# Optimization experiments

Hardware: AMD Instinct MI355X
Metric: run time of the kernel (lower is better)

The kernel has to match this reference:

```python
import jax, jax.numpy as jnp
import numpy as np

TAU1, TAU2, TSCALE = 30.0, 5.0, 6.0   # tau1 > tau2, in frame units (hz=None)
B, T_OUT = 1000, 20000                # neurons x output frames


def _biexp_kernel():
    # exact replica of SpikeToCalcium.set_double_exp
    r = TAU1 / TAU2
    d = TAU1 - TAU2
    scale = np.power(r, -TAU2 / d) - np.power(r, -TAU1 / d)
    t = np.arange(1.0, TAU1 * TSCALE + 2.0, dtype=np.float32)  # 181 taps
    e1 = np.exp(-t / TAU1)
    e2 = np.exp(-t / TAU2)
    return ((e1 - e2) / scale).astype(np.float32)


def setup_inputs() -> dict:
    key = jax.random.key(0)
    kernel = jnp.asarray(_biexp_kernel())           # (181,)
    Kt = kernel.shape[0]
    u = jax.random.normal(key, (B, T_OUT + Kt - 1), dtype=jnp.float32)  # (1000, 20180)
    return {"u": u, "kernel": kernel}


def reference(u, kernel):
    # Original: K.conv1d(u[..., None], kernel[::-1, None, None], 1, 'valid')
    # keras conv1d is cross-correlation; reversing the kernel makes it a true
    # causal FIR convolution. lax.conv_general_dilated is also cross-correlation,
    # so we pass the reversed kernel identically.
    rhs = kernel[::-1][None, None, :]               # (O=1, I=1, K)
    lhs = u[:, None, :]                             # (B, C=1, T_in)
    out = jax.lax.conv_general_dilated(
        lhs, rhs, window_strides=(1,), padding='VALID',
        dimension_numbers=('NCH', 'OIH', 'NCH'))
    return out[:, 0, :]                             # (B, T_in - K + 1)
```

## Files before the change

kernel.cpp:

```cpp
#include <hip/hip_runtime.h>
#include <math.h>


namespace {
constexpr int kB   = 1000;
constexpr int kT   = 20000;
constexpr int kInW = kT + 180;
constexpr int W    = 180;
constexpr int L    = 836;
constexpr int NCHK = 2;
}

struct Coefs {
  float r1e[8], r2e[8];
  float s1c[6], s2c[6];
  float r1_512;
  float A1, A1d, A2;
};

__global__ __launch_bounds__(256, 8)
void biexp_iir_scan(const float* __restrict__ u, float* __restrict__ out, Coefs cf) {
  const int lane = threadIdx.x & 63;
  const int seg  = (blockIdx.x << 2) | (threadIdx.x >> 6);
  const int row  = blockIdx.y;
  const int n0   = seg * L;
  const int nend = (n0 + L < kT) ? n0 + L : kT;
  const int lim  = nend - n0 + W;
  const float* ur = u + (size_t)row * kInW;
  float* outr = out + (size_t)row * kT;

  const int colbase = n0 + 8 * lane;
  int col0 = colbase;
  col0 = col0 < (kInW - 8) ? col0 : (kInW - 8);
  int col1 = colbase + 512;
  col1 = col1 < (kInW - 8) ? col1 : (kInW - 8);
  const float4 a0 = *(const float4*)(ur + col0);
  const float4 a1 = *(const float4*)(ur + col0 + 4);
  const float4 b0 = *(const float4*)(ur + col1);
  const float4 b1 = *(const float4*)(ur + col1 + 4);

  float r1l = 1.f, r2l = 1.f;
  #pragma unroll
  for (int i = 0; i < 6; ++i) {
    r1l *= (lane & (1 << i)) ? cf.s1c[i] : 1.f;
    r2l *= (lane & (1 << i)) ? cf.s2c[i] : 1.f;
  }

  float C1 = 0.f, C2 = 0.f;
  float pw[8];
  #pragma unroll
  for (int j = 0; j < 8; ++j) pw[j] = 0.f;

  auto chunk = [&](const float4& qa, const float4& qb, int c) {
    const float ux[8] = {qa.x, qa.y, qa.z, qa.w, qb.x, qb.y, qb.z, qb.w};

    float p1[8], p2[8];
    p1[0] = ux[0]; p2[0] = ux[0];
    #pragma unroll
    for (int j = 1; j < 8; ++j) {
      p1[j] = fmaf(cf.r1e[1], p1[j-1], ux[j]);
      p2[j] = fmaf(cf.r2e[1], p2[j-1], ux[j]);
    }

    float S1 = p1[7], S2 = p2[7], t;
    t = __shfl_up(S1, 1);  S1 = lane >= 1  ? fmaf(cf.s1c[0], t, S1) : S1;
    t = __shfl_up(S2, 1);  S2 = lane >= 1  ? fmaf(cf.s2c[0], t, S2) : S2;
    t = __shfl_up(S1, 2);  S1 = lane >= 2  ? fmaf(cf.s1c[1], t, S1) : S1;
    t = __shfl_up(S2, 2);  S2 = lane >= 2  ? fmaf(cf.s2c[1], t, S2) : S2;
    t = __shfl_up(S1, 4);  S1 = lane >= 4  ? fmaf(cf.s1c[2], t, S1) : S1;
    t = __shfl_up(S2, 4);  S2 = lane >= 4  ? fmaf(cf.s2c[2], t, S2) : S2;
    t = __shfl_up(S1, 8);  S1 = lane >= 8  ? fmaf(cf.s1c[3], t, S1) : S1;
    t = __shfl_up(S2, 8);  S2 = lane >= 8  ? fmaf(cf.s2c[3], t, S2) : S2;
    t = __shfl_up(S1, 16); S1 = lane >= 16 ? fmaf(cf.s1c[4], t, S1) : S1;
    t = __shfl_up(S1, 32); S1 = lane >= 32 ? fmaf(cf.s1c[5], t, S1) : S1;

    float X1 = __shfl_up(S1, 1); X1 = (lane == 0) ? 0.f : X1;
    float X2 = __shfl_up(S2, 1); X2 = (lane == 0) ? 0.f : X2;
    const float H1 = cf.r1e[1] * fmaf(r1l, C1, X1);
    const float H2 = cf.r2e[1] * fmaf(r2l, C2, X2);

    float s1[8], s2[8];
    #pragma unroll
    for (int j = 0; j < 8; ++j) {
      s1[j] = fmaf(cf.r1e[j], H1, p1[j]);
      s2[j] = fmaf(cf.r2e[j], H2, p2[j]);
    }
    C1 = fmaf(cf.r1_512, C1, __shfl(S1, 63));
    C2 = __shfl(S2, 63);

    float y[8];
    #pragma unroll
    for (int j = 0; j < 8; ++j) {
      const int slot = (j < 5) ? j + 3 : j - 5;
      const int rot  = (j < 5) ? 23 : 22;
      const float z  = (lane <= 63 - rot) ? s1[slot] : pw[slot];
      const float d  = __shfl(z, (lane - rot) & 63);
      y[j] = fmaf(-cf.A2, s2[j], fmaf(-cf.A1d, d, cf.A1 * s1[j]));
    }
    #pragma unroll
    for (int j = 0; j < 8; ++j) pw[j] = s1[j];

    const int off0 = (c << 9) + 8 * lane;
    if (off0 >= W && off0 < lim) {
      float4 v; v.x = y[0]; v.y = y[1]; v.z = y[2]; v.w = y[3];
      *(float4*)(outr + (n0 - W + off0)) = v;
    }
    if (off0 + 4 >= W && off0 + 4 < lim) {
      float4 v; v.x = y[4]; v.y = y[5]; v.z = y[6]; v.w = y[7];
      *(float4*)(outr + (n0 - W + off0 + 4)) = v;
    }
  };

  chunk(a0, a1, 0);
  chunk(b0, b1, 1);
}

extern "C" void kernel_launch(void* const* d_in, const int* in_sizes, int n_in,
                              void* d_out, int out_size, void* d_ws, size_t ws_size,
                              hipStream_t stream) {
  const float* u = (const float*)d_in[0];
  float* out = (float*)d_out;

  const double r1 = exp(-1.0 / 30.0);
  const double r2 = exp(-1.0 / 5.0);
  const double scale = pow(6.0, -5.0 / 25.0) - pow(6.0, -30.0 / 25.0);

  Coefs cf;
  for (int j = 0; j < 8; ++j) {
    cf.r1e[j] = (float)pow(r1, (double)j);
    cf.r2e[j] = (float)pow(r2, (double)j);
  }
  for (int i = 0; i < 6; ++i) {
    cf.s1c[i] = (float)pow(r1, (double)(8 << i));
    cf.s2c[i] = (float)pow(r2, (double)(8 << i));
  }
  cf.r1_512 = (float)pow(r1, 512.0);
  cf.A1  = (float)(r1 / scale);
  cf.A1d = (float)(pow(r1, 182.0) / scale);
  cf.A2  = (float)(r2 / scale);

  hipLaunchKernelGGL(biexp_iir_scan, dim3(6, kB), dim3(256, 1, 1), 0, stream,
                     u, out, cf);
}
```

Measured before the change: 142.4 us.

## Process one 1024-sample window per wave with 16 elements per lane

Each wave now loads 16 consecutive samples per lane and covers its whole segment window in one pass, replacing the two 8-element chunks with a carried prefix. The cross-lane scan shrinks to five levels for the slow pole and three for the fast pole. The delayed-tap lookup becomes a single rotated shuffle with zero fill, and the segment length is retuned. The aim is fewer shuffles and less carried state per output, at the cost of more registers per thread (launch bounds lowered to 6) and more overlap work since segment length and window ratio change.

```diff
diff --git a/kernel.cpp b/kernel.cpp
--- a/kernel.cpp
+++ b/kernel.cpp
@@ -7,18 +7,18 @@
 constexpr int kT   = 20000;
 constexpr int kInW = kT + 180;
 constexpr int W    = 180;
-constexpr int L    = 836;
-constexpr int NCHK = 2;
+constexpr int L    = 844;
+constexpr int SEGS = 24;
 }
 
 struct Coefs {
-  float r1e[8], r2e[8];
-  float s1c[6], s2c[6];
-  float r1_512;
+  float r1e[16], r2e[16];
+  float s1c[5];
+  float s2c[3];
   float A1, A1d, A2;
 };
 
-__global__ __launch_bounds__(256, 8)
+__global__ __launch_bounds__(256, 6)
 void biexp_iir_scan(const float* __restrict__ u, float* __restrict__ out, Coefs cf) {
   const int lane = threadIdx.x & 63;
   const int seg  = (blockIdx.x << 2) | (threadIdx.x >> 6);
@@ -29,90 +29,67 @@
   const float* ur = u + (size_t)row * kInW;
   float* outr = out + (size_t)row * kT;
 
-  const int colbase = n0 + 8 * lane;
-  int col0 = colbase;
-  col0 = col0 < (kInW - 8) ? col0 : (kInW - 8);
-  int col1 = colbase + 512;
-  col1 = col1 < (kInW - 8) ? col1 : (kInW - 8);
-  const float4 a0 = *(const float4*)(ur + col0);
-  const float4 a1 = *(const float4*)(ur + col0 + 4);
-  const float4 b0 = *(const float4*)(ur + col1);
-  const float4 b1 = *(const float4*)(ur + col1 + 4);
+  int cb = n0 + 16 * lane;
+  cb = cb < (kInW - 16) ? cb : (kInW - 16);
+  const float4 q0 = *(const float4*)(ur + cb);
+  const float4 q1 = *(const float4*)(ur + cb + 4);
+  const float4 q2 = *(const float4*)(ur + cb + 8);
+  const float4 q3 = *(const float4*)(ur + cb + 12);
 
-  float r1l = 1.f, r2l = 1.f;
+  const float ux[16] = {q0.x, q0.y, q0.z, q0.w, q1.x, q1.y, q1.z, q1.w,
+                        q2.x, q2.y, q2.z, q2.w, q3.x, q3.y, q3.z, q3.w};
+
+  float p1[16], p2[16];
+  p1[0] = ux[0]; p2[0] = ux[0];
   #pragma unroll
-  for (int i = 0; i < 6; ++i) {
-    r1l *= (lane & (1 << i)) ? cf.s1c[i] : 1.f;
-    r2l *= (lane & (1 << i)) ? cf.s2c[i] : 1.f;
+  for (int j = 1; j < 16; ++j) {
+    p1[j] = fmaf(cf.r1e[1], p1[j-1], ux[j]);
+    p2[j] = fmaf(cf.r2e[1], p2[j-1], ux[j]);
   }
 
-  float C1 = 0.f, C2 = 0.f;
-  float pw[8];
+  float S1 = p1[15], S2 = p2[15], t;
+  t = __shfl_up(S1, 1);  S1 = lane >= 1  ? fmaf(cf.s1c[0], t, S1) : S1;
+  t = __shfl_up(S2, 1);  S2 = lane >= 1  ? fmaf(cf.s2c[0], t, S2) : S2;
+  t = __shfl_up(S1, 2);  S1 = lane >= 2  ? fmaf(cf.s1c[1], t, S1) : S1;
+  t = __shfl_up(S2, 2);  S2 = lane >= 2  ? fmaf(cf.s2c[1], t, S2) : S2;
+  t = __shfl_up(S1, 4);  S1 = lane >= 4  ? fmaf(cf.s1c[2], t, S1) : S1;
+  t = __shfl_up(S2, 4);  S2 = lane >= 4  ? fmaf(cf.s2c[2], t, S2) : S2;
+  t = __shfl_up(S1, 8);  S1 = lane >= 8  ? fmaf(cf.s1c[3], t, S1) : S1;
+  t = __shfl_up(S1, 16); S1 = lane >= 16 ? fmaf(cf.s1c[4], t, S1) : S1;
+
+  float X1 = __shfl_up(S1, 1); X1 = (lane == 0) ? 0.f : X1;
+  float X2 = __shfl_up(S2, 1); X2 = (lane == 0) ? 0.f : X2;
+  const float H1 = cf.r1e[1] * X1;
+  const float H2 = cf.r2e[1] * X2;
+
+  float s1[16], s2[16];
   #pragma unroll
-  for (int j = 0; j < 8; ++j) pw[j] = 0.f;
+  for (int j = 0; j < 16; ++j) {
+    s1[j] = fmaf(cf.r1e[j], H1, p1[j]);
+    s2[j] = fmaf(cf.r2e[j], H2, p2[j]);
+  }
 
-  auto chunk = [&](const float4& qa, const float4& qb, int c) {
-    const float ux[8] = {qa.x, qa.y, qa.z, qa.w, qb.x, qb.y, qb.z, qb.w};
+  float y[16];
+  #pragma unroll
+  for (int j = 0; j < 16; ++j) {
+    const int slot = (j >= 5) ? j - 5 : j + 11;
+    const int rot  = (j >= 5) ? 11 : 12;
+    const float zz = __shfl(s1[slot], (lane - rot) & 63);
+    const float d  = (lane >= rot) ? zz : 0.f;
+    y[j] = fmaf(-cf.A2, s2[j], fmaf(-cf.A1d, d, cf.A1 * s1[j]));
+  }
 
-    float p1[8], p2[8];
-    p1[0] = ux[0]; p2[0] = ux[0];
-    #pragma unroll
-    for (int j = 1; j < 8; ++j) {
-      p1[j] = fmaf(cf.r1e[1], p1[j-1], ux[j]);
-      p2[j] = fmaf(cf.r2e[1], p2[j-1], ux[j]);
+  const int off0 = 16 * lane;
+  float* op = outr + (n0 - W + off0);
+  #pragma unroll
+  for (int q = 0; q < 4; ++q) {
+    const int off = off0 + 4 * q;
+    if (off >= W && off < lim) {
+      float4 v;
+      v.x = y[4*q+0]; v.y = y[4*q+1]; v.z = y[4*q+2]; v.w = y[4*q+3];
+      *(float4*)(op + 4 * q) = v;
     }
-
-    float S1 = p1[7], S2 = p2[7], t;
-    t = __shfl_up(S1, 1);  S1 = lane >= 1  ? fmaf(cf.s1c[0], t, S1) : S1;
-    t = __shfl_up(S2, 1);  S2 = lane >= 1  ? fmaf(cf.s2c[0], t, S2) : S2;
-    t = __shfl_up(S1, 2);  S1 = lane >= 2  ? fmaf(cf.s1c[1], t, S1) : S1;
-    t = __shfl_up(S2, 2);  S2 = lane >= 2  ? fmaf(cf.s2c[1], t, S2) : S2;
-    t = __shfl_up(S1, 4);  S1 = lane >= 4  ? fmaf(cf.s1c[2], t, S1) : S1;
-    t = __shfl_up(S2, 4);  S2 = lane >= 4  ? fmaf(cf.s2c[2], t, S2) : S2;
-    t = __shfl_up(S1, 8);  S1 = lane >= 8  ? fmaf(cf.s1c[3], t, S1) : S1;
-    t = __shfl_up(S2, 8);  S2 = lane >= 8  ? fmaf(cf.s2c[3], t, S2) : S2;
-    t = __shfl_up(S1, 16); S1 = lane >= 16 ? fmaf(cf.s1c[4], t, S1) : S1;
-    t = __shfl_up(S1, 32); S1 = lane >= 32 ? fmaf(cf.s1c[5], t, S1) : S1;
-
-    float X1 = __shfl_up(S1, 1); X1 = (lane == 0) ? 0.f : X1;
-    float X2 = __shfl_up(S2, 1); X2 = (lane == 0) ? 0.f : X2;
-    const float H1 = cf.r1e[1] * fmaf(r1l, C1, X1);
-    const float H2 = cf.r2e[1] * fmaf(r2l, C2, X2);
-
-    float s1[8], s2[8];
-    #pragma unroll
-    for (int j = 0; j < 8; ++j) {
-      s1[j] = fmaf(cf.r1e[j], H1, p1[j]);
-      s2[j] = fmaf(cf.r2e[j], H2, p2[j]);
-    }
-    C1 = fmaf(cf.r1_512, C1, __shfl(S1, 63));
-    C2 = __shfl(S2, 63);
-
-    float y[8];
-    #pragma unroll
-    for (int j = 0; j < 8; ++j) {
-      const int slot = (j < 5) ? j + 3 : j - 5;
-      const int rot  = (j < 5) ? 23 : 22;
-      const float z  = (lane <= 63 - rot) ? s1[slot] : pw[slot];
-      const float d  = __shfl(z, (lane - rot) & 63);
-      y[j] = fmaf(-cf.A2, s2[j], fmaf(-cf.A1d, d, cf.A1 * s1[j]));
-    }
-    #pragma unroll
-    for (int j = 0; j < 8; ++j) pw[j] = s1[j];
-
-    const int off0 = (c << 9) + 8 * lane;
-    if (off0 >= W && off0 < lim) {
-      float4 v; v.x = y[0]; v.y = y[1]; v.z = y[2]; v.w = y[3];
-      *(float4*)(outr + (n0 - W + off0)) = v;
-    }
-    if (off0 + 4 >= W && off0 + 4 < lim) {
-      float4 v; v.x = y[4]; v.y = y[5]; v.z = y[6]; v.w = y[7];
-      *(float4*)(outr + (n0 - W + off0 + 4)) = v;
-    }
-  };
-
-  chunk(a0, a1, 0);
-  chunk(b0, b1, 1);
+  }
 }
 
 extern "C" void kernel_launch(void* const* d_in, const int* in_sizes, int n_in,
@@ -126,19 +103,16 @@
   const double scale = pow(6.0, -5.0 / 25.0) - pow(6.0, -30.0 / 25.0);
 
   Coefs cf;
-  for (int j = 0; j < 8; ++j) {
+  for (int j = 0; j < 16; ++j) {
     cf.r1e[j] = (float)pow(r1, (double)j);
     cf.r2e[j] = (float)pow(r2, (double)j);
   }
-  for (int i = 0; i < 6; ++i) {
-    cf.s1c[i] = (float)pow(r1, (double)(8 << i));
-    cf.s2c[i] = (float)pow(r2, (double)(8 << i));
-  }
-  cf.r1_512 = (float)pow(r1, 512.0);
+  for (int i = 0; i < 5; ++i) cf.s1c[i] = (float)pow(r1, (double)(16 << i));
+  for (int i = 0; i < 3; ++i) cf.s2c[i] = (float)pow(r2, (double)(16 << i));
   cf.A1  = (float)(r1 / scale);
   cf.A1d = (float)(pow(r1, 182.0) / scale);
   cf.A2  = (float)(r2 / scale);
 
-  hipLaunchKernelGGL(biexp_iir_scan, dim3(6, kB), dim3(256, 1, 1), 0, stream,
+  hipLaunchKernelGGL(biexp_iir_scan, dim3(SEGS / 4, kB), dim3(256, 1, 1), 0, stream,
                      u, out, cf);
 }
```

Result: slower. 150.9 us (+6.0%).

## Use persistent waves with next-task load prefetch and XCD-aware block remap

Applied to the files above, without the earlier changes.

Swaps the one-segment-per-wave 2D grid for a fixed grid of 2048 blocks. Each wave loops over up to three (row, segment) tasks and issues the global loads for the next task before computing the current one, with a sched_barrier to keep that ordering. Block indices are also permuted so consecutive logical blocks land across the XCDs. The goal is to hide global-load latency in this latency-bound scan, at the cost of more live registers and uneven tail work across waves.

```diff
diff --git a/kernel.cpp b/kernel.cpp
--- a/kernel.cpp
+++ b/kernel.cpp
@@ -3,12 +3,15 @@
 
 
 namespace {
-constexpr int kB   = 1000;
-constexpr int kT   = 20000;
-constexpr int kInW = kT + 180;
-constexpr int W    = 180;
-constexpr int L    = 836;
-constexpr int NCHK = 2;
+constexpr int kB    = 1000;
+constexpr int kT    = 20000;
+constexpr int kInW  = kT + 180;
+constexpr int W     = 180;
+constexpr int L     = 836;
+constexpr int SEGS  = 24;
+constexpr int NTASK = SEGS * kB;
+constexpr int NBLK  = 2048;
+constexpr int NWAVE = NBLK * 4;
 }
 
 struct Coefs {
@@ -21,23 +24,9 @@
 __global__ __launch_bounds__(256, 8)
 void biexp_iir_scan(const float* __restrict__ u, float* __restrict__ out, Coefs cf) {
   const int lane = threadIdx.x & 63;
-  const int seg  = (blockIdx.x << 2) | (threadIdx.x >> 6);
-  const int row  = blockIdx.y;
-  const int n0   = seg * L;
-  const int nend = (n0 + L < kT) ? n0 + L : kT;
-  const int lim  = nend - n0 + W;
-  const float* ur = u + (size_t)row * kInW;
-  float* outr = out + (size_t)row * kT;
 
-  const int colbase = n0 + 8 * lane;
-  int col0 = colbase;
-  col0 = col0 < (kInW - 8) ? col0 : (kInW - 8);
-  int col1 = colbase + 512;
-  col1 = col1 < (kInW - 8) ? col1 : (kInW - 8);
-  const float4 a0 = *(const float4*)(ur + col0);
-  const float4 a1 = *(const float4*)(ur + col0 + 4);
-  const float4 b0 = *(const float4*)(ur + col1);
-  const float4 b1 = *(const float4*)(ur + col1 + 4);
+  const int lbid = (blockIdx.x & 7) * (NBLK >> 3) + (blockIdx.x >> 3);
+  const int w    = (lbid << 2) | (threadIdx.x >> 6);
 
   float r1l = 1.f, r2l = 1.f;
   #pragma unroll
@@ -46,73 +35,114 @@
     r2l *= (lane & (1 << i)) ? cf.s2c[i] : 1.f;
   }
 
-  float C1 = 0.f, C2 = 0.f;
-  float pw[8];
-  #pragma unroll
-  for (int j = 0; j < 8; ++j) pw[j] = 0.f;
+  auto load_task = [&](int t, float4& a0, float4& a1, float4& b0, float4& b1) {
+    const int row = t / SEGS;
+    const int n0  = (t - row * SEGS) * L;
+    const float* ur = u + (size_t)row * kInW;
+    int c0 = n0 + 8 * lane;
+    c0 = c0 < (kInW - 8) ? c0 : (kInW - 8);
+    int c1 = n0 + 512 + 8 * lane;
+    c1 = c1 < (kInW - 8) ? c1 : (kInW - 8);
+    a0 = *(const float4*)(ur + c0);
+    a1 = *(const float4*)(ur + c0 + 4);
+    b0 = *(const float4*)(ur + c1);
+    b1 = *(const float4*)(ur + c1 + 4);
+  };
 
-  auto chunk = [&](const float4& qa, const float4& qb, int c) {
-    const float ux[8] = {qa.x, qa.y, qa.z, qa.w, qb.x, qb.y, qb.z, qb.w};
+  auto compute_store = [&](int t, const float4& qa0, const float4& qa1,
+                                  const float4& qb0, const float4& qb1) {
+    const int row  = t / SEGS;
+    const int n0   = (t - row * SEGS) * L;
+    const int nend = (n0 + L < kT) ? n0 + L : kT;
+    const int lim  = nend - n0 + W;
+    float* outr = out + (size_t)row * kT;
 
-    float p1[8], p2[8];
-    p1[0] = ux[0]; p2[0] = ux[0];
+    float C1 = 0.f, C2 = 0.f;
+    float pw[8];
     #pragma unroll
-    for (int j = 1; j < 8; ++j) {
-      p1[j] = fmaf(cf.r1e[1], p1[j-1], ux[j]);
-      p2[j] = fmaf(cf.r2e[1], p2[j-1], ux[j]);
-    }
+    for (int j = 0; j < 8; ++j) pw[j] = 0.f;
 
-    float S1 = p1[7], S2 = p2[7], t;
-    t = __shfl_up(S1, 1);  S1 = lane >= 1  ? fmaf(cf.s1c[0], t, S1) : S1;
-    t = __shfl_up(S2, 1);  S2 = lane >= 1  ? fmaf(cf.s2c[0], t, S2) : S2;
-    t = __shfl_up(S1, 2);  S1 = lane >= 2  ? fmaf(cf.s1c[1], t, S1) : S1;
-    t = __shfl_up(S2, 2);  S2 = lane >= 2  ? fmaf(cf.s2c[1], t, S2) : S2;
-    t = __shfl_up(S1, 4);  S1 = lane >= 4  ? fmaf(cf.s1c[2], t, S1) : S1;
-    t = __shfl_up(S2, 4);  S2 = lane >= 4  ? fmaf(cf.s2c[2], t, S2) : S2;
-    t = __shfl_up(S1, 8);  S1 = lane >= 8  ? fmaf(cf.s1c[3], t, S1) : S1;
-    t = __shfl_up(S2, 8);  S2 = lane >= 8  ? fmaf(cf.s2c[3], t, S2) : S2;
-    t = __shfl_up(S1, 16); S1 = lane >= 16 ? fmaf(cf.s1c[4], t, S1) : S1;
-    t = __shfl_up(S1, 32); S1 = lane >= 32 ? fmaf(cf.s1c[5], t, S1) : S1;
+    #pragma unroll
+    for (int c = 0; c < 2; ++c) {
+      const float4& qa = c ? qb0 : qa0;
+      const float4& qb = c ? qb1 : qa1;
+      const float ux[8] = {qa.x, qa.y, qa.z, qa.w, qb.x, qb.y, qb.z, qb.w};
 
-    float X1 = __shfl_up(S1, 1); X1 = (lane == 0) ? 0.f : X1;
-    float X2 = __shfl_up(S2, 1); X2 = (lane == 0) ? 0.f : X2;
-    const float H1 = cf.r1e[1] * fmaf(r1l, C1, X1);
-    const float H2 = cf.r2e[1] * fmaf(r2l, C2, X2);
+      float p1[8], p2[8];
+      p1[0] = ux[0]; p2[0] = ux[0];
+      #pragma unroll
+      for (int j = 1; j < 8; ++j) {
+        p1[j] = fmaf(cf.r1e[1], p1[j-1], ux[j]);
+        p2[j] = fmaf(cf.r2e[1], p2[j-1], ux[j]);
+      }
 
-    float s1[8], s2[8];
-    #pragma unroll
-    for (int j = 0; j < 8; ++j) {
-      s1[j] = fmaf(cf.r1e[j], H1, p1[j]);
-      s2[j] = fmaf(cf.r2e[j], H2, p2[j]);
-    }
-    C1 = fmaf(cf.r1_512, C1, __shfl(S1, 63));
-    C2 = __shfl(S2, 63);
+      float S1 = p1[7], S2 = p2[7], t_;
+      t_ = __shfl_up(S1, 1);  S1 = lane >= 1  ? fmaf(cf.s1c[0], t_, S1) : S1;
+      t_ = __shfl_up(S2, 1);  S2 = lane >= 1  ? fmaf(cf.s2c[0], t_, S2) : S2;
+      t_ = __shfl_up(S1, 2);  S1 = lane >= 2  ? fmaf(cf.s1c[1], t_, S1) : S1;
+      t_ = __shfl_up(S2, 2);  S2 = lane >= 2  ? fmaf(cf.s2c[1], t_, S2) : S2;
+      t_ = __shfl_up(S1, 4);  S1 = lane >= 4  ? fmaf(cf.s1c[2], t_, S1) : S1;
+      t_ = __shfl_up(S2, 4);  S2 = lane >= 4  ? fmaf(cf.s2c[2], t_, S2) : S2;
+      t_ = __shfl_up(S1, 8);  S1 = lane >= 8  ? fmaf(cf.s1c[3], t_, S1) : S1;
+      t_ = __shfl_up(S2, 8);  S2 = lane >= 8  ? fmaf(cf.s2c[3], t_, S2) : S2;
+      t_ = __shfl_up(S1, 16); S1 = lane >= 16 ? fmaf(cf.s1c[4], t_, S1) : S1;
+      t_ = __shfl_up(S1, 32); S1 = lane >= 32 ? fmaf(cf.s1c[5], t_, S1) : S1;
 
-    float y[8];
-    #pragma unroll
-    for (int j = 0; j < 8; ++j) {
-      const int slot = (j < 5) ? j + 3 : j - 5;
-      const int rot  = (j < 5) ? 23 : 22;
-      const float z  = (lane <= 63 - rot) ? s1[slot] : pw[slot];
-      const float d  = __shfl(z, (lane - rot) & 63);
-      y[j] = fmaf(-cf.A2, s2[j], fmaf(-cf.A1d, d, cf.A1 * s1[j]));
-    }
-    #pragma unroll
-    for (int j = 0; j < 8; ++j) pw[j] = s1[j];
+      float X1 = __shfl_up(S1, 1); X1 = (lane == 0) ? 0.f : X1;
+      float X2 = __shfl_up(S2, 1); X2 = (lane == 0) ? 0.f : X2;
+      const float H1 = cf.r1e[1] * fmaf(r1l, C1, X1);
+      const float H2 = cf.r2e[1] * fmaf(r2l, C2, X2);
 
-    const int off0 = (c << 9) + 8 * lane;
-    if (off0 >= W && off0 < lim) {
-      float4 v; v.x = y[0]; v.y = y[1]; v.z = y[2]; v.w = y[3];
-      *(float4*)(outr + (n0 - W + off0)) = v;
-    }
-    if (off0 + 4 >= W && off0 + 4 < lim) {
-      float4 v; v.x = y[4]; v.y = y[5]; v.z = y[6]; v.w = y[7];
-      *(float4*)(outr + (n0 - W + off0 + 4)) = v;
+      float s1[8], s2[8];
+      #pragma unroll
+      for (int j = 0; j < 8; ++j) {
+        s1[j] = fmaf(cf.r1e[j], H1, p1[j]);
+        s2[j] = fmaf(cf.r2e[j], H2, p2[j]);
+      }
+      C1 = fmaf(cf.r1_512, C1, __shfl(S1, 63));
+      C2 = __shfl(S2, 63);
+
+      float y[8];
+      #pragma unroll
+      for (int j = 0; j < 8; ++j) {
+        const int slot = (j < 5) ? j + 3 : j - 5;
+        const int rot  = (j < 5) ? 23 : 22;
+        const float z  = (lane <= 63 - rot) ? s1[slot] : pw[slot];
+        const float d  = __shfl(z, (lane - rot) & 63);
+        y[j] = fmaf(-cf.A2, s2[j], fmaf(-cf.A1d, d, cf.A1 * s1[j]));
+      }
+      #pragma unroll
+      for (int j = 0; j < 8; ++j) pw[j] = s1[j];
+
+      const int off0 = (c << 9) + 8 * lane;
+      if (off0 >= W && off0 < lim) {
+        float4 v; v.x = y[0]; v.y = y[1]; v.z = y[2]; v.w = y[3];
+        *(float4*)(outr + (n0 - W + off0)) = v;
+      }
+      if (off0 + 4 >= W && off0 + 4 < lim) {
+        float4 v; v.x = y[4]; v.y = y[5]; v.z = y[6]; v.w = y[7];
+        *(float4*)(outr + (n0 - W + off0 + 4)) = v;
+      }
     }
   };
 
-  chunk(a0, a1, 0);
-  chunk(b0, b1, 1);
+  int t = w;
+  float4 A0, A1v, B0, B1;
+  load_task(t, A0, A1v, B0, B1);
+
+  #pragma unroll
+  for (int i = 0; i < 3; ++i) {
+    if (i > 0 && t >= NTASK) break;
+    const int tn = t + NWAVE;
+    float4 P0, P1, P2, P3;
+    if (i < 2) {
+      const int tl = (tn < NTASK) ? tn : t;
+      load_task(tl, P0, P1, P2, P3);
+      __builtin_amdgcn_sched_barrier(0);
+    }
+    compute_store(t, A0, A1v, B0, B1);
+    if (i < 2) { A0 = P0; A1v = P1; B0 = P2; B1 = P3; t = tn; }
+  }
 }
 
 extern "C" void kernel_launch(void* const* d_in, const int* in_sizes, int n_in,
@@ -139,6 +169,6 @@
   cf.A1d = (float)(pow(r1, 182.0) / scale);
   cf.A2  = (float)(r2 / scale);
 
-  hipLaunchKernelGGL(biexp_iir_scan, dim3(6, kB), dim3(256, 1, 1), 0, stream,
+  hipLaunchKernelGGL(biexp_iir_scan, dim3(NBLK), dim3(256, 1, 1), 0, stream,
                      u, out, cf);
 }
```

After: 176.2 us. +23.8%, slower.
